# Kernel tuning notes

Hardware: AMD Instinct MI355X
Metric: run time of the kernel (lower is better)

## Reference

```python
import jax, jax.numpy as jnp
import numpy as np

N = 50000
E = 800000
H = 96
NUM_IN = 11
PE_DIM = 24
NUM_OUT = 1
NUM_LAYERS = 4
NUM_GRAPHS = 256


def _linear_params(key, d_in, d_out):
    k1, k2 = jax.random.split(key)
    bound = 1.0 / np.sqrt(d_in)
    w = jax.random.uniform(k1, (d_in, d_out), jnp.float32, -bound, bound)
    b = jax.random.uniform(k2, (d_out,), jnp.float32, -bound, bound)
    return w, b


def setup_inputs() -> dict:
    key = jax.random.key(0)
    ks = jax.random.split(key, 32)
    x = jax.random.normal(ks[0], (N, NUM_IN), jnp.float32)
    pos = jax.random.normal(ks[1], (N, 3), jnp.float32)
    pe = jax.random.normal(ks[2], (N, PE_DIM), jnp.float32)
    edge_index = jax.random.randint(ks[3], (2, E), 0, N, jnp.int64)
    batch = jnp.sort(jax.random.randint(ks[4], (N,), 0, NUM_GRAPHS, jnp.int64))
    embed_w1, embed_b1 = _linear_params(ks[5], NUM_IN + PE_DIM, H)
    embed_w2, embed_b2 = _linear_params(ks[6], H, H)
    # per-layer stacked params
    msg_w1 = []; msg_b1 = []; msg_w2 = []; msg_b2 = []
    upd_w1 = []; upd_b1 = []; upd_w2 = []; upd_b2 = []
    for l in range(NUM_LAYERS):
        w, b = _linear_params(ks[7 + l], 2 * H + 1, H); msg_w1.append(w); msg_b1.append(b)
        w, b = _linear_params(ks[11 + l], H, H); msg_w2.append(w); msg_b2.append(b)
        w, b = _linear_params(ks[15 + l], 2 * H, H); upd_w1.append(w); upd_b1.append(b)
        w, b = _linear_params(ks[19 + l], H, H); upd_w2.append(w); upd_b2.append(b)
    pre_w1, pre_b1 = _linear_params(ks[23], H, H)
    pre_w2, pre_b2 = _linear_params(ks[24], H, H)
    ro_w1, ro_b1 = _linear_params(ks[25], H, H)
    ro_w2, ro_b2 = _linear_params(ks[26], H, NUM_OUT)
    return {
        'x': x, 'pos': pos, 'pe': pe, 'edge_index': edge_index, 'batch': batch,
        'embed_w1': embed_w1, 'embed_b1': embed_b1, 'embed_w2': embed_w2, 'embed_b2': embed_b2,
        'msg_w1': jnp.stack(msg_w1), 'msg_b1': jnp.stack(msg_b1),
        'msg_w2': jnp.stack(msg_w2), 'msg_b2': jnp.stack(msg_b2),
        'upd_w1': jnp.stack(upd_w1), 'upd_b1': jnp.stack(upd_b1),
        'upd_w2': jnp.stack(upd_w2), 'upd_b2': jnp.stack(upd_b2),
        'pre_w1': pre_w1, 'pre_b1': pre_b1, 'pre_w2': pre_w2, 'pre_b2': pre_b2,
        'ro_w1': ro_w1, 'ro_b1': ro_b1, 'ro_w2': ro_w2, 'ro_b2': ro_b2,
    }


def _egnn_forward(x, pos, pe, edge_index, batch,
                  embed_w1, embed_b1, embed_w2, embed_b2,
                  msg_w1, msg_b1, msg_w2, msg_b2,
                  upd_w1, upd_b1, upd_w2, upd_b2,
                  pre_w1, pre_b1, pre_w2, pre_b2,
                  ro_w1, ro_b1, ro_w2, ro_b2):
    silu = jax.nn.silu
    send, rec = edge_index[0], edge_index[1]
    h = jnp.concatenate([x, pe], axis=-1)
    h = silu(h @ embed_w1 + embed_b1) @ embed_w2 + embed_b2  # [N,H]
    dist = jnp.linalg.norm(pos[send] - pos[rec], axis=1)[:, None]  # [E,1]
    for l in range(NUM_LAYERS):
        state = jnp.concatenate([h[send], h[rec], dist], axis=1)  # [E,2H+1]
        msg = silu(silu(state @ msg_w1[l] + msg_b1[l]) @ msg_w2[l] + msg_b2[l])  # [E,H]
        aggr = jax.ops.segment_sum(msg, rec, num_segments=h.shape[0])  # [N,H]
        upd_in = jnp.concatenate([h, aggr], axis=1)
        update = silu(upd_in @ upd_w1[l] + upd_b1[l]) @ upd_w2[l] + upd_b2[l]
        h = h + update
    h = silu(h @ pre_w1 + pre_b1) @ pre_w2 + pre_b2
    pooled = jax.ops.segment_sum(h, batch, num_segments=NUM_GRAPHS)  # [G,H]
    out = silu(pooled @ ro_w1 + ro_b1) @ ro_w2 + ro_b2  # [G,1]
    return jnp.squeeze(out)


def reference(x, pos, pe, edge_index, batch,
              embed_w1, embed_b1, embed_w2, embed_b2,
              msg_w1, msg_b1, msg_w2, msg_b2,
              upd_w1, upd_b1, upd_w2, upd_b2,
              pre_w1, pre_b1, pre_w2, pre_b2,
              ro_w1, ro_b1, ro_w2, ro_b2):
    return _egnn_forward(x, pos, pe, edge_index, batch,
                         embed_w1, embed_b1, embed_w2, embed_b2,
                         msg_w1, msg_b1, msg_w2, msg_b2,
                         upd_w1, upd_b1, upd_w2, upd_b2,
                         pre_w1, pre_b1, pre_w2, pre_b2,
                         ro_w1, ro_b1, ro_w2, ro_b2)
```

## Files before the change

kernel.cpp:

```cpp
#include <hip/hip_runtime.h>
#include <hip/hip_bf16.h>

#define HDIM 96
#define TILE 128
#define NTILE 64

typedef __attribute__((ext_vector_type(8))) short  short8;
typedef __attribute__((ext_vector_type(4))) short  short4v;
typedef __attribute__((ext_vector_type(4))) float  float4v;
typedef __attribute__((ext_vector_type(4))) unsigned int uint4v;

static __device__ __forceinline__ short f2bf(float f){
    unsigned u = __float_as_uint(f);
    return (short)((u + 0x8000u) >> 16);
}
static __device__ __forceinline__ float bf2f(short s){
    unsigned u = ((unsigned)(unsigned short)s) << 16;
    return __uint_as_float(u);
}
static __device__ __forceinline__ float silu_f(float v){
    return v * __builtin_amdgcn_rcpf(1.0f + __expf(-v));
}

struct SwJob { const float* src; int ck; int ks; int ksrc; };
struct SwTable { SwJob j[22]; };

__global__ __launch_bounds__(256) void swizzle_kernel(SwTable T, short* __restrict__ dst, int total){
    int gid = blockIdx.x*256 + threadIdx.x;
    if (gid >= total) return;
    int ksg = gid / 3072;
    int e   = gid % 3072;
    const float* src = T.j[0].src; int k0 = 0, ksrc = 0;
    #pragma unroll
    for (int jj = 0; jj < 22; ++jj){
        int s = T.j[jj].ck;
        if (ksg >= s && ksg < s + T.j[jj].ks){ src = T.j[jj].src; k0 = (ksg - s)*32; ksrc = T.j[jj].ksrc; }
    }
    int nt   = e >> 9;
    int rem  = e & 511;
    int lane = rem >> 3;
    int jx   = rem & 7;
    int k = k0 + ((lane >> 4) << 3) + jx;
    int f = nt*16 + (lane & 15);
    float v = (k < ksrc) ? src[(size_t)k*HDIM + f] : 0.0f;
    dst[gid] = f2bf(v);
}

__global__ __launch_bounds__(256) void swizzle2_kernel(const float* __restrict__ msg_w1,
                                                       short* __restrict__ dst, int total){
    int gid = blockIdx.x*256 + threadIdx.x;
    if (gid >= total) return;
    int layer = gid / 18432;
    int e     = gid % 18432;
    int ksg = e / 6144;
    int rem = e % 6144;
    int nt   = rem >> 9;
    int r2   = rem & 511;
    int lane = r2 >> 3;
    int jx   = r2 & 7;
    int k = ksg*32 + ((lane >> 4) << 3) + jx;
    int f = nt*16 + (lane & 15);
    int row = (f < 96) ? k : (96 + k);
    int col = (f < 96) ? f : (f - 96);
    dst[gid] = f2bf(msg_w1[(size_t)layer*193*96 + (size_t)row*96 + col]);
}

__global__ __launch_bounds__(256) void hist_kernel(const int* __restrict__ rec, int* __restrict__ deg, int E){
    int e = blockIdx.x*256 + threadIdx.x;
    if (e < E) atomicAdd(&deg[rec[e]], 1);
}

__global__ __launch_bounds__(256) void scan_part(const int* __restrict__ deg, int* __restrict__ part, int N){
    __shared__ int red[256];
    const int t = threadIdx.x;
    int base = blockIdx.x*1024;
    int s = 0;
    #pragma unroll
    for (int j=0;j<4;j++){ int i = base + j*256 + t; s += (i<N)?deg[i]:0; }
    red[t]=s; __syncthreads();
    #pragma unroll
    for (int off=128; off>0; off>>=1){ if (t<off) red[t]+=red[t+off]; __syncthreads(); }
    if (t==0) part[blockIdx.x]=red[0];
}
__global__ __launch_bounds__(256) void scan_top(int* __restrict__ part, int nb){
    __shared__ int buf[256];
    const int t = threadIdx.x;
    int v = (t < nb) ? part[t] : 0;
    buf[t] = v;
    __syncthreads();
    #pragma unroll
    for (int off=1; off<256; off<<=1){
        int u = (t>=off)?buf[t-off]:0;
        __syncthreads();
        buf[t] += u;
        __syncthreads();
    }
    if (t < nb) part[t] = buf[t] - v;
}
__global__ __launch_bounds__(256) void scan_final(const int* __restrict__ deg, const int* __restrict__ part,
                                                  int* __restrict__ cur, int N){
    __shared__ int tsum[256];
    const int t = threadIdx.x;
    int i0 = blockIdx.x*1024 + t*4;
    int a0 = (i0+0<N)?deg[i0+0]:0;
    int a1 = (i0+1<N)?deg[i0+1]:0;
    int a2 = (i0+2<N)?deg[i0+2]:0;
    int a3 = (i0+3<N)?deg[i0+3]:0;
    int s = a0+a1+a2+a3;
    tsum[t]=s; __syncthreads();
    #pragma unroll
    for (int off=1; off<256; off<<=1){
        int u = (t>=off)?tsum[t-off]:0;
        __syncthreads();
        tsum[t]+=u;
        __syncthreads();
    }
    int excl = tsum[t]-s + part[blockIdx.x];
    if (i0+0<N) cur[i0+0]=excl;
    if (i0+1<N) cur[i0+1]=excl+a0;
    if (i0+2<N) cur[i0+2]=excl+a0+a1;
    if (i0+3<N) cur[i0+3]=excl+a0+a1+a2;
}

__global__ __launch_bounds__(256) void scatter_kernel(
    const int* __restrict__ send, const int* __restrict__ rec, const float* __restrict__ pos,
    int* __restrict__ cur, int2* __restrict__ sd_s, int* __restrict__ rec_s, int E)
{
    int e = blockIdx.x*256 + threadIdx.x;
    if (e >= E) return;
    int s = send[e], r = rec[e];
    int p = atomicAdd(&cur[r], 1);
    float dx = pos[3*s]   - pos[3*r];
    float dy = pos[3*s+1] - pos[3*r+1];
    float dz = pos[3*s+2] - pos[3*r+2];
    float d = sqrtf(dx*dx + dy*dy + dz*dz);
    sd_s[p] = make_int2(s, __float_as_int(d));
    rec_s[p] = r;
}

__global__ __launch_bounds__(256,5) void edge_kernel(
    const short* __restrict__ SR,
    const int2* __restrict__ sd_s, const int* __restrict__ rec_s,
    const float* __restrict__ w1r192,
    const short* __restrict__ w2sw, const float* __restrict__ b2,
    float* __restrict__ aggr, int E)
{
    __shared__ short msgS[TILE*104];
    __shared__ int   recS[TILE];
    __shared__ int   startIdxS[TILE+1];
    __shared__ int   wcntS[2];
    const int t  = threadIdx.x;
    const int e0 = blockIdx.x * TILE;

    if (t < TILE) {
        int e = e0 + t; if (e >= E) e = E - 1;
        recS[t] = rec_s[e];
    }
    __syncthreads();

    bool flag = false;
    if (t < TILE) flag = (t == 0) || (recS[t] != recS[t-1]);
    unsigned long long bmask = __ballot(flag ? 1 : 0);
    int pre = __popcll(bmask & ((1ull << (t & 63)) - 1ull));
    if (t < TILE && (t & 63) == 0) wcntS[t >> 6] = __popcll(bmask);
    __syncthreads();
    const int nseg = wcntS[0] + wcntS[1];
    if (flag) startIdxS[pre + ((t >> 6) ? wcntS[0] : 0)] = t;
    if (t == 0) startIdxS[nseg] = TILE;

    const bool firstB = (e0 > 0) && (rec_s[e0-1] == recS[0]);
    const bool lastB  = (e0 + TILE < E) && (rec_s[e0 + TILE] == recS[TILE-1]);

    const int lane = t & 63;
    const int wv   = t >> 6;
    const int e_lo = wv * 32;
    const int col  = lane & 15;
    const int quad = lane >> 4;
    const int frow = quad * 4;
    const float4v fzero = {0.f,0.f,0.f,0.f};

    short8 frag[2][3];
    #pragma unroll
    for (int et=0; et<2; ++et){
        int ei = e_lo + et*16 + col;
        int ec = e0 + ei; if (ec >= E) ec = E - 1;
        int2 sd = sd_s[ec];
        int se = sd.x;
        float d = __int_as_float(sd.y);
        int re = recS[ei];
        #pragma unroll
        for (int ks=0; ks<3; ++ks){
            int f0 = ks*32 + quad*8;
            short8 S8 = *(const short8*)(SR + (size_t)se*192 + f0);
            short8 R8 = *(const short8*)(SR + (size_t)re*192 + 96 + f0);
            float4v wa = *(const float4v*)(w1r192 + f0);
            float4v wb = *(const float4v*)(w1r192 + f0 + 4);
            short8 fr;
            #pragma unroll
            for (int j=0;j<8;j++){
                float w = (j<4) ? wa[j] : wb[j-4];
                float v = bf2f(S8[j]) + bf2f(R8[j]) + d*w;
                fr[j] = f2bf(silu_f(v));
            }
            frag[et][ks] = fr;
        }
    }

    float4v acc2[2][6];
    #pragma unroll
    for (int i=0;i<2;i++)
      #pragma unroll
      for (int n=0;n<6;n++) acc2[i][n] = fzero;

    const short8* w2f = (const short8*)w2sw;
    #pragma unroll
    for (int ks = 0; ks < 3; ++ks) {
        #pragma unroll
        for (int mt = 0; mt < 6; ++mt) {
            short8 a = w2f[(ks*6+mt)*64 + lane];
            acc2[0][mt] = __builtin_amdgcn_mfma_f32_16x16x32_bf16(a, frag[0][ks], acc2[0][mt], 0, 0, 0);
            acc2[1][mt] = __builtin_amdgcn_mfma_f32_16x16x32_bf16(a, frag[1][ks], acc2[1][mt], 0, 0, 0);
        }
    }
    float4v b2v[6];
    #pragma unroll
    for (int mt=0; mt<6; ++mt) b2v[mt] = *(const float4v*)(b2 + mt*16 + frow);

    #pragma unroll
    for (int et=0; et<2; ++et){
        int e = e_lo + et*16 + col;
        bool valid = (e0 + e) < E;
        #pragma unroll
        for (int mt=0; mt<6; ++mt){
            short4v sv;
            #pragma unroll
            for (int r=0;r<4;r++){
                float u = silu_f(acc2[et][mt][r] + b2v[mt][r]);
                sv[r] = f2bf(valid ? u : 0.0f);
            }
            *(short4v*)(msgS + e*104 + mt*16 + frow) = sv;
        }
    }
    __syncthreads();

    const int items = nseg * 12;
    for (int item = t; item < items; item += 256){
        int s  = item / 12;
        int fg = item - s*12;
        int r0 = startIdxS[s], r1 = startIdxS[s+1];
        float sum[8] = {0.f,0.f,0.f,0.f,0.f,0.f,0.f,0.f};
        for (int r = r0; r < r1; ++r){
            short8 v8 = *(const short8*)(msgS + r*104 + fg*8);
            #pragma unroll
            for (int j=0;j<8;j++) sum[j] += bf2f(v8[j]);
        }
        float* dstp = aggr + (size_t)recS[r0]*HDIM + fg*8;
        bool bnd = (s == 0 && firstB) || (s == nseg-1 && lastB);
        if (bnd) {
            #pragma unroll
            for (int j=0;j<8;j++) atomicAdd(dstp+j, sum[j]);
        } else {
            float4v lo = {sum[0], sum[1], sum[2], sum[3]};
            float4v hi = {sum[4], sum[5], sum[6], sum[7]};
            *(float4v*)(dstp)     = lo;
            *(float4v*)(dstp + 4) = hi;
        }
    }
}

__global__ __launch_bounds__(128,3) void update_kernel(
    float* __restrict__ h, short* __restrict__ hbf, float* __restrict__ aggr,
    const short* __restrict__ w1sw, const float* __restrict__ b1,
    const short* __restrict__ w2sw, const float* __restrict__ b2,
    const short* __restrict__ w1sr_next, const float* __restrict__ msgb1_next,
    short* __restrict__ SR, int N)
{
    __shared__ short stateS[NTILE*200];
    const int t  = threadIdx.x;
    const int n0 = blockIdx.x * NTILE;

    #pragma unroll
    for (int it = 0; it < 12; ++it) {
        int q = it*128 + t;
        int c = q % 24;
        int i = q / 24;
        int node = n0 + i;
        if (c < 12) {
            uint4v v = {0u,0u,0u,0u};
            if (node < N) v = *(const uint4v*)(hbf + (size_t)node*HDIM + c*8);
            *(uint4v*)(stateS + i*200 + c*8) = v;
        } else {
            int cc = c - 12;
            short8 s8 = {0,0,0,0,0,0,0,0};
            if (node < N) {
                float4v a0 = *(const float4v*)(aggr + (size_t)node*HDIM + cc*8);
                float4v a1 = *(const float4v*)(aggr + (size_t)node*HDIM + cc*8 + 4);
                s8[0]=f2bf(a0[0]); s8[1]=f2bf(a0[1]); s8[2]=f2bf(a0[2]); s8[3]=f2bf(a0[3]);
                s8[4]=f2bf(a1[0]); s8[5]=f2bf(a1[1]); s8[6]=f2bf(a1[2]); s8[7]=f2bf(a1[3]);
            }
            *(short8*)(stateS + i*200 + HDIM + cc*8) = s8;
        }
    }
    __syncthreads();

    const int lane = t & 63;
    const int wv   = t >> 6;
    const int e_lo = wv * 32;
    const int col  = lane & 15;
    const int quad = lane >> 4;
    const int koff = quad * 8;
    const int frow = quad * 4;
    const float4v fzero = {0.f,0.f,0.f,0.f};

    float4v acc[2][6];
    #pragma unroll
    for (int i=0;i<2;i++)
      #pragma unroll
      for (int n=0;n<6;n++) acc[i][n] = fzero;

    const short8* w1f = (const short8*)w1sw;
    #pragma unroll
    for (int ks = 0; ks < 6; ++ks) {
        short8 bb0 = *(const short8*)(stateS + (e_lo+col)*200    + ks*32 + koff);
        short8 bb1 = *(const short8*)(stateS + (e_lo+16+col)*200 + ks*32 + koff);
        #pragma unroll
        for (int mt = 0; mt < 6; ++mt) {
            short8 a = w1f[(ks*6+mt)*64 + lane];
            acc[0][mt] = __builtin_amdgcn_mfma_f32_16x16x32_bf16(a, bb0, acc[0][mt], 0, 0, 0);
            acc[1][mt] = __builtin_amdgcn_mfma_f32_16x16x32_bf16(a, bb1, acc[1][mt], 0, 0, 0);
        }
    }
    float4v b1v[6];
    #pragma unroll
    for (int mt=0; mt<6; ++mt) b1v[mt] = *(const float4v*)(b1 + mt*16 + frow);
    __syncthreads();

    short* t1S = stateS;
    #pragma unroll
    for (int et=0; et<2; ++et){
        int e = e_lo + et*16 + col;
        #pragma unroll
        for (int mt=0; mt<6; ++mt){
            short4v sv;
            #pragma unroll
            for (int r=0;r<4;r++) sv[r] = f2bf(silu_f(acc[et][mt][r] + b1v[mt][r]));
            *(short4v*)(t1S + e*104 + mt*16 + frow) = sv;
        }
    }
    __syncthreads();

    float4v acc2[2][6];
    #pragma unroll
    for (int i=0;i<2;i++)
      #pragma unroll
      for (int n=0;n<6;n++) acc2[i][n] = fzero;

    const short8* w2f = (const short8*)w2sw;
    #pragma unroll
    for (int ks = 0; ks < 3; ++ks) {
        short8 bb0 = *(const short8*)(t1S + (e_lo+col)*104    + ks*32 + koff);
        short8 bb1 = *(const short8*)(t1S + (e_lo+16+col)*104 + ks*32 + koff);
        #pragma unroll
        for (int mt = 0; mt < 6; ++mt) {
            short8 a = w2f[(ks*6+mt)*64 + lane];
            acc2[0][mt] = __builtin_amdgcn_mfma_f32_16x16x32_bf16(a, bb0, acc2[0][mt], 0, 0, 0);
            acc2[1][mt] = __builtin_amdgcn_mfma_f32_16x16x32_bf16(a, bb1, acc2[1][mt], 0, 0, 0);
        }
    }
    float4v b2v[6];
    #pragma unroll
    for (int mt=0; mt<6; ++mt) b2v[mt] = *(const float4v*)(b2 + mt*16 + frow);
    __syncthreads();

    #pragma unroll
    for (int et=0; et<2; ++et){
        int erow = e_lo + et*16 + col;
        int node = n0 + erow;
        bool valid = node < N;
        size_t base = (size_t)node*HDIM;
        #pragma unroll
        for (int mt=0; mt<6; ++mt){
            int f0 = mt*16 + frow;
            float4v old = valid ? *(const float4v*)(h + base + f0) : fzero;
            float4v o;
            #pragma unroll
            for (int r=0;r<4;r++) o[r] = old[r] + acc2[et][mt][r] + b2v[mt][r];
            short4v sv = {f2bf(o[0]), f2bf(o[1]), f2bf(o[2]), f2bf(o[3])};
            if (valid) {
                *(float4v*)(h + base + f0) = o;
                *(short4v*)(hbf + base + f0) = sv;
                *(float4v*)(aggr + base + f0) = fzero;
            }
            *(short4v*)(stateS + erow*104 + f0) = sv;
        }
    }

    if (w1sr_next) {
        __syncthreads();
        float4v accS[2][12];
        #pragma unroll
        for (int i=0;i<2;i++)
          #pragma unroll
          for (int n=0;n<12;n++) accS[i][n] = fzero;

        const short8* wsf = (const short8*)w1sr_next;
        #pragma unroll
        for (int ks = 0; ks < 3; ++ks) {
            short8 bb0 = *(const short8*)(stateS + (e_lo+col)*104    + ks*32 + koff);
            short8 bb1 = *(const short8*)(stateS + (e_lo+16+col)*104 + ks*32 + koff);
            #pragma unroll
            for (int mt = 0; mt < 12; ++mt) {
                short8 a = wsf[(ks*12+mt)*64 + lane];
                accS[0][mt] = __builtin_amdgcn_mfma_f32_16x16x32_bf16(a, bb0, accS[0][mt], 0, 0, 0);
                accS[1][mt] = __builtin_amdgcn_mfma_f32_16x16x32_bf16(a, bb1, accS[1][mt], 0, 0, 0);
            }
        }
        float4v bnv[6];
        #pragma unroll
        for (int mt=0; mt<6; ++mt) bnv[mt] = *(const float4v*)(msgb1_next + mt*16 + frow);

        #pragma unroll
        for (int et=0; et<2; ++et){
            int node = n0 + e_lo + et*16 + col;
            if (node < N) {
                size_t sbase = (size_t)node*192;
                #pragma unroll
                for (int mt=0; mt<12; ++mt){
                    float4v o = accS[et][mt];
                    if (mt < 6) { o[0]+=bnv[mt][0]; o[1]+=bnv[mt][1]; o[2]+=bnv[mt][2]; o[3]+=bnv[mt][3]; }
                    short4v sv = {f2bf(o[0]), f2bf(o[1]), f2bf(o[2]), f2bf(o[3])};
                    *(short4v*)(SR + sbase + mt*16 + frow) = sv;
                }
            }
        }
    }
}

__global__ __launch_bounds__(128,3) void embed_kernel(
    const float* __restrict__ x, const float* __restrict__ pe,
    const short* __restrict__ w1sw, const float* __restrict__ b1,
    const short* __restrict__ w2sw, const float* __restrict__ b2,
    float* __restrict__ h, short* __restrict__ hbf,
    const short* __restrict__ w1sr0, const float* __restrict__ msgb1_0,
    short* __restrict__ SR, int N)
{
    __shared__ short stateS[NTILE*72];
    __shared__ short t1S[NTILE*104];
    const int t  = threadIdx.x;
    const int n0 = blockIdx.x * NTILE;

    if (t < NTILE) {
        int node = n0 + t;
        short* row = stateS + t*72;
        if (node < N) {
            #pragma unroll
            for (int j=0;j<11;j++) row[j]    = f2bf(x[(size_t)node*11 + j]);
            #pragma unroll
            for (int j=0;j<24;j++) row[11+j] = f2bf(pe[(size_t)node*24 + j]);
            #pragma unroll
            for (int j=35;j<64;j++) row[j] = 0;
        } else {
            #pragma unroll
            for (int j=0;j<64;j++) row[j] = 0;
        }
    }
    __syncthreads();

    const int lane = t & 63;
    const int wv   = t >> 6;
    const int e_lo = wv * 32;
    const int col  = lane & 15;
    const int quad = lane >> 4;
    const int koff = quad * 8;
    const int frow = quad * 4;
    const float4v fzero = {0.f,0.f,0.f,0.f};

    float4v acc[2][6];
    #pragma unroll
    for (int i=0;i<2;i++)
      #pragma unroll
      for (int n=0;n<6;n++) acc[i][n] = fzero;

    const short8* w1f = (const short8*)w1sw;
    #pragma unroll
    for (int ks = 0; ks < 2; ++ks) {
        short8 bb0 = *(const short8*)(stateS + (e_lo+col)*72    + ks*32 + koff);
        short8 bb1 = *(const short8*)(stateS + (e_lo+16+col)*72 + ks*32 + koff);
        #pragma unroll
        for (int mt = 0; mt < 6; ++mt) {
            short8 a = w1f[(ks*6+mt)*64 + lane];
            acc[0][mt] = __builtin_amdgcn_mfma_f32_16x16x32_bf16(a, bb0, acc[0][mt], 0, 0, 0);
            acc[1][mt] = __builtin_amdgcn_mfma_f32_16x16x32_bf16(a, bb1, acc[1][mt], 0, 0, 0);
        }
    }
    float4v b1v[6];
    #pragma unroll
    for (int mt=0; mt<6; ++mt) b1v[mt] = *(const float4v*)(b1 + mt*16 + frow);

    #pragma unroll
    for (int et=0; et<2; ++et){
        int e = e_lo + et*16 + col;
        #pragma unroll
        for (int mt=0; mt<6; ++mt){
            short4v sv;
            #pragma unroll
            for (int r=0;r<4;r++) sv[r] = f2bf(silu_f(acc[et][mt][r] + b1v[mt][r]));
            *(short4v*)(t1S + e*104 + mt*16 + frow) = sv;
        }
    }
    __syncthreads();

    float4v acc2[2][6];
    #pragma unroll
    for (int i=0;i<2;i++)
      #pragma unroll
      for (int n=0;n<6;n++) acc2[i][n] = fzero;

    const short8* w2f = (const short8*)w2sw;
    #pragma unroll
    for (int ks = 0; ks < 3; ++ks) {
        short8 bb0 = *(const short8*)(t1S + (e_lo+col)*104    + ks*32 + koff);
        short8 bb1 = *(const short8*)(t1S + (e_lo+16+col)*104 + ks*32 + koff);
        #pragma unroll
        for (int mt = 0; mt < 6; ++mt) {
            short8 a = w2f[(ks*6+mt)*64 + lane];
            acc2[0][mt] = __builtin_amdgcn_mfma_f32_16x16x32_bf16(a, bb0, acc2[0][mt], 0, 0, 0);
            acc2[1][mt] = __builtin_amdgcn_mfma_f32_16x16x32_bf16(a, bb1, acc2[1][mt], 0, 0, 0);
        }
    }
    float4v b2v[6];
    #pragma unroll
    for (int mt=0; mt<6; ++mt) b2v[mt] = *(const float4v*)(b2 + mt*16 + frow);
    __syncthreads();

    #pragma unroll
    for (int et=0; et<2; ++et){
        int erow = e_lo + et*16 + col;
        int node = n0 + erow;
        bool valid = node < N;
        size_t base = (size_t)node*HDIM;
        #pragma unroll
        for (int mt=0; mt<6; ++mt){
            int f0 = mt*16 + frow;
            float4v o;
            #pragma unroll
            for (int r=0;r<4;r++) o[r] = acc2[et][mt][r] + b2v[mt][r];
            short4v sv = {f2bf(o[0]), f2bf(o[1]), f2bf(o[2]), f2bf(o[3])};
            if (valid) {
                *(float4v*)(h + base + f0) = o;
                *(short4v*)(hbf + base + f0) = sv;
            }
            *(short4v*)(t1S + erow*104 + f0) = sv;
        }
    }
    __syncthreads();

    float4v accS[2][12];
    #pragma unroll
    for (int i=0;i<2;i++)
      #pragma unroll
      for (int n=0;n<12;n++) accS[i][n] = fzero;

    const short8* wsf = (const short8*)w1sr0;
    #pragma unroll
    for (int ks = 0; ks < 3; ++ks) {
        short8 bb0 = *(const short8*)(t1S + (e_lo+col)*104    + ks*32 + koff);
        short8 bb1 = *(const short8*)(t1S + (e_lo+16+col)*104 + ks*32 + koff);
        #pragma unroll
        for (int mt = 0; mt < 12; ++mt) {
            short8 a = wsf[(ks*12+mt)*64 + lane];
            accS[0][mt] = __builtin_amdgcn_mfma_f32_16x16x32_bf16(a, bb0, accS[0][mt], 0, 0, 0);
            accS[1][mt] = __builtin_amdgcn_mfma_f32_16x16x32_bf16(a, bb1, accS[1][mt], 0, 0, 0);
        }
    }
    float4v bnv[6];
    #pragma unroll
    for (int mt=0; mt<6; ++mt) bnv[mt] = *(const float4v*)(msgb1_0 + mt*16 + frow);

    #pragma unroll
    for (int et=0; et<2; ++et){
        int node = n0 + e_lo + et*16 + col;
        if (node < N) {
            size_t sbase = (size_t)node*192;
            #pragma unroll
            for (int mt=0; mt<12; ++mt){
                float4v o = accS[et][mt];
                if (mt < 6) { o[0]+=bnv[mt][0]; o[1]+=bnv[mt][1]; o[2]+=bnv[mt][2]; o[3]+=bnv[mt][3]; }
                short4v sv = {f2bf(o[0]), f2bf(o[1]), f2bf(o[2]), f2bf(o[3])};
                *(short4v*)(SR + sbase + mt*16 + frow) = sv;
            }
        }
    }
}

__global__ __launch_bounds__(128,3) void prepool_kernel(
    const short* __restrict__ hbf,
    const short* __restrict__ w1sw, const float* __restrict__ b1,
    const short* __restrict__ w2sw, const float* __restrict__ b2,
    const int* __restrict__ batch, float* __restrict__ pooled, int N)
{
    __shared__ short bufS[NTILE*104*2];
    __shared__ int   batchS[NTILE];
    __shared__ int   startIdxS[NTILE+1];
    __shared__ int   nsegS;
    short* stateS = bufS;
    short* t1S    = bufS + NTILE*104;
    float* msgS   = (float*)bufS;
    const int t  = threadIdx.x;
    const int n0 = blockIdx.x * NTILE;

    #pragma unroll
    for (int it = 0; it < 6; ++it) {
        int q = it*128 + t;
        int c = q % 12;
        int i = q / 12;
        int node = n0 + i;
        uint4v v = {0u,0u,0u,0u};
        if (node < N) v = *(const uint4v*)(hbf + (size_t)node*HDIM + c*8);
        *(uint4v*)(stateS + i*104 + c*8) = v;
    }
    if (t < NTILE) {
        int node = n0 + t;
        batchS[t] = batch[node < N ? node : N-1];
    }
    __syncthreads();

    bool flag = false;
    if (t < NTILE) flag = (t == 0) || (batchS[t] != batchS[t-1]);
    unsigned long long bmask = __ballot(flag ? 1 : 0);
    if (t < NTILE) {
        int pre = __popcll(bmask & ((1ull << t) - 1ull));
        if (flag) startIdxS[pre] = t;
        if (t == 0) nsegS = __popcll(bmask);
    }

    const int lane = t & 63;
    const int wv   = t >> 6;
    const int e_lo = wv * 32;
    const int col  = lane & 15;
    const int quad = lane >> 4;
    const int koff = quad * 8;
    const int frow = quad * 4;
    const float4v fzero = {0.f,0.f,0.f,0.f};

    float4v acc[2][6];
    #pragma unroll
    for (int i=0;i<2;i++)
      #pragma unroll
      for (int n=0;n<6;n++) acc[i][n] = fzero;

    const short8* w1f = (const short8*)w1sw;
    #pragma unroll
    for (int ks = 0; ks < 3; ++ks) {
        short8 bb0 = *(const short8*)(stateS + (e_lo+col)*104    + ks*32 + koff);
        short8 bb1 = *(const short8*)(stateS + (e_lo+16+col)*104 + ks*32 + koff);
        #pragma unroll
        for (int mt = 0; mt < 6; ++mt) {
            short8 a = w1f[(ks*6+mt)*64 + lane];
            acc[0][mt] = __builtin_amdgcn_mfma_f32_16x16x32_bf16(a, bb0, acc[0][mt], 0, 0, 0);
            acc[1][mt] = __builtin_amdgcn_mfma_f32_16x16x32_bf16(a, bb1, acc[1][mt], 0, 0, 0);
        }
    }
    float4v b1v[6];
    #pragma unroll
    for (int mt=0; mt<6; ++mt) b1v[mt] = *(const float4v*)(b1 + mt*16 + frow);

    #pragma unroll
    for (int et=0; et<2; ++et){
        int e = e_lo + et*16 + col;
        #pragma unroll
        for (int mt=0; mt<6; ++mt){
            short4v sv;
            #pragma unroll
            for (int r=0;r<4;r++) sv[r] = f2bf(silu_f(acc[et][mt][r] + b1v[mt][r]));
            *(short4v*)(t1S + e*104 + mt*16 + frow) = sv;
        }
    }
    __syncthreads();
    const int nseg = nsegS;
    if (t == 0) startIdxS[nseg] = NTILE;

    float4v acc2[2][6];
    #pragma unroll
    for (int i=0;i<2;i++)
      #pragma unroll
      for (int n=0;n<6;n++) acc2[i][n] = fzero;

    const short8* w2f = (const short8*)w2sw;
    #pragma unroll
    for (int ks = 0; ks < 3; ++ks) {
        short8 bb0 = *(const short8*)(t1S + (e_lo+col)*104    + ks*32 + koff);
        short8 bb1 = *(const short8*)(t1S + (e_lo+16+col)*104 + ks*32 + koff);
        #pragma unroll
        for (int mt = 0; mt < 6; ++mt) {
            short8 a = w2f[(ks*6+mt)*64 + lane];
            acc2[0][mt] = __builtin_amdgcn_mfma_f32_16x16x32_bf16(a, bb0, acc2[0][mt], 0, 0, 0);
            acc2[1][mt] = __builtin_amdgcn_mfma_f32_16x16x32_bf16(a, bb1, acc2[1][mt], 0, 0, 0);
        }
    }
    float4v b2v[6];
    #pragma unroll
    for (int mt=0; mt<6; ++mt) b2v[mt] = *(const float4v*)(b2 + mt*16 + frow);
    __syncthreads();

    #pragma unroll
    for (int et=0; et<2; ++et){
        int e = e_lo + et*16 + col;
        bool valid = (n0 + e) < N;
        #pragma unroll
        for (int mt=0; mt<6; ++mt){
            float4v v;
            #pragma unroll
            for (int r=0;r<4;r++){
                float u = acc2[et][mt][r] + b2v[mt][r];
                v[r] = valid ? u : 0.0f;
            }
            *(float4v*)(msgS + e*100 + mt*16 + frow) = v;
        }
    }
    __syncthreads();

    const int items = nseg * 24;
    for (int item = t; item < items; item += 128){
        int s  = item / 24;
        int fg = item - s*24;
        int r0 = startIdxS[s], r1 = startIdxS[s+1];
        float4v sum = fzero;
        for (int r = r0; r < r1; ++r) sum += *(const float4v*)(msgS + r*100 + fg*4);
        float* dstp = pooled + (size_t)batchS[r0]*HDIM + fg*4;
        atomicAdd(dstp+0, sum[0]);
        atomicAdd(dstp+1, sum[1]);
        atomicAdd(dstp+2, sum[2]);
        atomicAdd(dstp+3, sum[3]);
    }
}

__global__ __launch_bounds__(128) void readout_kernel(
    const float* __restrict__ pooled,
    const float* __restrict__ w1, const float* __restrict__ b1,
    const float* __restrict__ w2, const float* __restrict__ b2,
    float* __restrict__ out)
{
    __shared__ float red[128];
    const int g = blockIdx.x;
    const int t = threadIdx.x;
    float p = 0.0f;
    if (t < HDIM) {
        float acc = b1[t];
        for (int k = 0; k < HDIM; ++k)
            acc += pooled[(size_t)g*HDIM + k] * w1[(size_t)k*HDIM + t];
        acc = silu_f(acc);
        p = acc * w2[t];
    }
    red[t] = p;
    __syncthreads();
    for (int s = 64; s > 0; s >>= 1) {
        if (t < s) red[t] += red[t + s];
        __syncthreads();
    }
    if (t == 0) out[g] = red[0] + b2[0];
}

extern "C" void kernel_launch(void* const* d_in, const int* in_sizes, int n_in,
                              void* d_out, int out_size, void* d_ws, size_t ws_size,
                              hipStream_t stream)
{
    const float* x        = (const float*)d_in[0];
    const float* pos      = (const float*)d_in[1];
    const float* pe       = (const float*)d_in[2];
    const int*   ei       = (const int*)d_in[3];
    const int*   batch    = (const int*)d_in[4];
    const float* embed_w1 = (const float*)d_in[5];
    const float* embed_b1 = (const float*)d_in[6];
    const float* embed_w2 = (const float*)d_in[7];
    const float* embed_b2 = (const float*)d_in[8];
    const float* msg_w1   = (const float*)d_in[9];
    const float* msg_b1   = (const float*)d_in[10];
    const float* msg_w2   = (const float*)d_in[11];
    const float* msg_b2   = (const float*)d_in[12];
    const float* upd_w1   = (const float*)d_in[13];
    const float* upd_b1   = (const float*)d_in[14];
    const float* upd_w2   = (const float*)d_in[15];
    const float* upd_b2   = (const float*)d_in[16];
    const float* pre_w1   = (const float*)d_in[17];
    const float* pre_b1   = (const float*)d_in[18];
    const float* pre_w2   = (const float*)d_in[19];
    const float* pre_b2   = (const float*)d_in[20];
    const float* ro_w1    = (const float*)d_in[21];
    const float* ro_b1    = (const float*)d_in[22];
    const float* ro_w2    = (const float*)d_in[23];
    const float* ro_b2    = (const float*)d_in[24];

    const int E = in_sizes[3] / 2;
    const int N = in_sizes[4];
    const int G = out_size;

    char* ws = (char*)d_ws;
    size_t off = 0;
    auto alloc = [&](size_t bytes){ void* p = ws + off; off += (bytes + 255) & ~(size_t)255; return p; };
    float* h      = (float*)alloc((size_t)N*HDIM*4);
    short* hbf    = (short*)alloc((size_t)N*HDIM*2);
    float* aggr   = (float*)alloc((size_t)N*HDIM*4);
    float* pooled = (float*)alloc((size_t)G*HDIM*4);
    short* wsw    = (short*)alloc((size_t)59*3072*2);
    short* w1sr   = (short*)alloc((size_t)4*18432*2);
    short* SR     = (short*)alloc((size_t)N*192*2);
    int*   deg    = (int*)alloc((size_t)N*4);
    int*   cur    = (int*)alloc((size_t)N*4);
    int*   part   = (int*)alloc((size_t)256*4);
    int2*  sd_s   = (int2*)alloc((size_t)E*8);
    int*   rec_s  = (int*)alloc((size_t)E*4);

    hipMemsetAsync(aggr,   0, (size_t)N*HDIM*4, stream);
    hipMemsetAsync(pooled, 0, (size_t)G*HDIM*4, stream);
    hipMemsetAsync(deg,    0, (size_t)N*4, stream);

    SwTable T;
    for (int jj=0;jj<22;jj++){ T.j[jj].src = embed_w1; T.j[jj].ck = 1<<30; T.j[jj].ks = 0; T.j[jj].ksrc = 0; }
    int ck = 0, ji = 0;
    auto add = [&](const float* s, int ks, int ksrc){
        T.j[ji].src = s; T.j[ji].ck = ck; T.j[ji].ks = ks; T.j[ji].ksrc = ksrc;
        ji++; ck += ks;
    };
    add(embed_w1, 2, 35);
    add(embed_w2, 3, 96);
    add(pre_w1,   3, 96);
    add(pre_w2,   3, 96);
    for (int l=0;l<4;l++) add(msg_w2 + (size_t)l*96*96,  3, 96);
    for (int l=0;l<4;l++) add(upd_w1 + (size_t)l*192*96, 6, 192);
    for (int l=0;l<4;l++) add(upd_w2 + (size_t)l*96*96,  3, 96);
    const int total = 59*3072;
    swizzle_kernel<<<(total+255)/256, 256, 0, stream>>>(T, wsw, total);
    const int total2 = 4*18432;
    swizzle2_kernel<<<(total2+255)/256, 256, 0, stream>>>(msg_w1, w1sr, total2);

    const int nbE256 = (E + 255) / 256;
    const int nbScan = (N + 1023) / 1024;
    hist_kernel<<<nbE256, 256, 0, stream>>>(ei + E, deg, E);
    scan_part<<<nbScan, 256, 0, stream>>>(deg, part, N);
    scan_top<<<1, 256, 0, stream>>>(part, nbScan);
    scan_final<<<nbScan, 256, 0, stream>>>(deg, part, cur, N);
    scatter_kernel<<<nbE256, 256, 0, stream>>>(ei, ei + E, pos, cur, sd_s, rec_s, E);

    const int nbN = (N + NTILE - 1) / NTILE;
    embed_kernel<<<nbN, 128, 0, stream>>>(x, pe, wsw + 0, embed_b1, wsw + 2*3072, embed_b2,
                                          h, hbf, w1sr, msg_b1, SR, N);

    const int nbE = (E + TILE - 1) / TILE;
    for (int l = 0; l < 4; ++l) {
        edge_kernel<<<nbE, 256, 0, stream>>>(SR, sd_s, rec_s,
            msg_w1 + (size_t)l*193*96 + (size_t)192*96,
            wsw + (11 + 3*l)*3072, msg_b2 + l*96, aggr, E);
        const short* w1sr_next = (l < 3) ? (w1sr + (size_t)(l+1)*18432) : nullptr;
        const float* msgb1_next = (l < 3) ? (msg_b1 + (l+1)*96) : nullptr;
        update_kernel<<<nbN, 128, 0, stream>>>(h, hbf, aggr,
            wsw + (23 + 6*l)*3072, upd_b1 + l*96,
            wsw + (47 + 3*l)*3072, upd_b2 + l*96,
            w1sr_next, msgb1_next, SR, N);
    }

    prepool_kernel<<<nbN, 128, 0, stream>>>(hbf, wsw + 5*3072, pre_b1, wsw + 8*3072, pre_b2,
                                            batch, pooled, N);
    readout_kernel<<<G, 128, 0, stream>>>(pooled, ro_w1, ro_b1, ro_w2, ro_b2, (float*)d_out);
}
```

Measured before the change: 803.0 us.

## Fuse prepool into last update kernel, merge swizzles, prefetch edge gathers early

Folds the pre-pooling MLP and the graph segment-sum into the last layer's update kernel, so the final node state never goes back to memory and one launch is removed. The two weight-swizzle kernels are merged into a single launch. The edge kernel now issues its sender and receiver feature gathers before the segment-boundary setup and its barrier, so those loads can overlap with that work. In exchange the update kernel uses more shared memory and registers, which may lower its occupancy in every layer.

```diff
diff --git a/kernel.cpp b/kernel.cpp
--- a/kernel.cpp
+++ b/kernel.cpp
@@ -25,44 +25,43 @@
 struct SwJob { const float* src; int ck; int ks; int ksrc; };
 struct SwTable { SwJob j[22]; };
 
-__global__ __launch_bounds__(256) void swizzle_kernel(SwTable T, short* __restrict__ dst, int total){
+__global__ __launch_bounds__(256) void swizzle_all(SwTable T, const float* __restrict__ msg_w1,
+                                                   short* __restrict__ dst, short* __restrict__ dst2,
+                                                   int total1, int total2){
     int gid = blockIdx.x*256 + threadIdx.x;
-    if (gid >= total) return;
-    int ksg = gid / 3072;
-    int e   = gid % 3072;
-    const float* src = T.j[0].src; int k0 = 0, ksrc = 0;
-    #pragma unroll
-    for (int jj = 0; jj < 22; ++jj){
-        int s = T.j[jj].ck;
-        if (ksg >= s && ksg < s + T.j[jj].ks){ src = T.j[jj].src; k0 = (ksg - s)*32; ksrc = T.j[jj].ksrc; }
-    }
-    int nt   = e >> 9;
-    int rem  = e & 511;
-    int lane = rem >> 3;
-    int jx   = rem & 7;
-    int k = k0 + ((lane >> 4) << 3) + jx;
-    int f = nt*16 + (lane & 15);
-    float v = (k < ksrc) ? src[(size_t)k*HDIM + f] : 0.0f;
-    dst[gid] = f2bf(v);
-}
-
-__global__ __launch_bounds__(256) void swizzle2_kernel(const float* __restrict__ msg_w1,
-                                                       short* __restrict__ dst, int total){
-    int gid = blockIdx.x*256 + threadIdx.x;
-    if (gid >= total) return;
-    int layer = gid / 18432;
-    int e     = gid % 18432;
-    int ksg = e / 6144;
-    int rem = e % 6144;
-    int nt   = rem >> 9;
-    int r2   = rem & 511;
-    int lane = r2 >> 3;
-    int jx   = r2 & 7;
-    int k = ksg*32 + ((lane >> 4) << 3) + jx;
-    int f = nt*16 + (lane & 15);
-    int row = (f < 96) ? k : (96 + k);
-    int col = (f < 96) ? f : (f - 96);
-    dst[gid] = f2bf(msg_w1[(size_t)layer*193*96 + (size_t)row*96 + col]);
+    if (gid < total1) {
+        int ksg = gid / 3072;
+        int e   = gid % 3072;
+        const float* src = T.j[0].src; int k0 = 0, ksrc = 0;
+        #pragma unroll
+        for (int jj = 0; jj < 22; ++jj){
+            int s = T.j[jj].ck;
+            if (ksg >= s && ksg < s + T.j[jj].ks){ src = T.j[jj].src; k0 = (ksg - s)*32; ksrc = T.j[jj].ksrc; }
+        }
+        int nt   = e >> 9;
+        int rem  = e & 511;
+        int lane = rem >> 3;
+        int jx   = rem & 7;
+        int k = k0 + ((lane >> 4) << 3) + jx;
+        int f = nt*16 + (lane & 15);
+        float v = (k < ksrc) ? src[(size_t)k*HDIM + f] : 0.0f;
+        dst[gid] = f2bf(v);
+    } else if (gid < total1 + total2) {
+        int g2 = gid - total1;
+        int layer = g2 / 18432;
+        int e     = g2 % 18432;
+        int ksg = e / 6144;
+        int rem = e % 6144;
+        int nt   = rem >> 9;
+        int r2   = rem & 511;
+        int lane = r2 >> 3;
+        int jx   = r2 & 7;
+        int k = ksg*32 + ((lane >> 4) << 3) + jx;
+        int f = nt*16 + (lane & 15);
+        int row = (f < 96) ? k : (96 + k);
+        int col = (f < 96) ? f : (f - 96);
+        dst2[g2] = f2bf(msg_w1[(size_t)layer*193*96 + (size_t)row*96 + col]);
+    }
 }
 
 __global__ __launch_bounds__(256) void hist_kernel(const int* __restrict__ rec, int* __restrict__ deg, int E){
@@ -151,26 +150,6 @@
     __shared__ int   wcntS[2];
     const int t  = threadIdx.x;
     const int e0 = blockIdx.x * TILE;
-
-    if (t < TILE) {
-        int e = e0 + t; if (e >= E) e = E - 1;
-        recS[t] = rec_s[e];
-    }
-    __syncthreads();
-
-    bool flag = false;
-    if (t < TILE) flag = (t == 0) || (recS[t] != recS[t-1]);
-    unsigned long long bmask = __ballot(flag ? 1 : 0);
-    int pre = __popcll(bmask & ((1ull << (t & 63)) - 1ull));
-    if (t < TILE && (t & 63) == 0) wcntS[t >> 6] = __popcll(bmask);
-    __syncthreads();
-    const int nseg = wcntS[0] + wcntS[1];
-    if (flag) startIdxS[pre + ((t >> 6) ? wcntS[0] : 0)] = t;
-    if (t == 0) startIdxS[nseg] = TILE;
-
-    const bool firstB = (e0 > 0) && (rec_s[e0-1] == recS[0]);
-    const bool lastB  = (e0 + TILE < E) && (rec_s[e0 + TILE] == recS[TILE-1]);
-
     const int lane = t & 63;
     const int wv   = t >> 6;
     const int e_lo = wv * 32;
@@ -179,22 +158,55 @@
     const int frow = quad * 4;
     const float4v fzero = {0.f,0.f,0.f,0.f};
 
+    int se[2], re[2]; float dd[2];
+    #pragma unroll
+    for (int et=0; et<2; ++et){
+        int ec = e0 + e_lo + et*16 + col; if (ec >= E) ec = E - 1;
+        int2 sd = sd_s[ec];
+        se[et] = sd.x; dd[et] = __int_as_float(sd.y);
+        re[et] = rec_s[ec];
+    }
+    short8 Sv[2][3], Rv[2][3];
+    #pragma unroll
+    for (int et=0; et<2; ++et)
+      #pragma unroll
+      for (int ks=0; ks<3; ++ks){
+        int f0 = ks*32 + quad*8;
+        Sv[et][ks] = *(const short8*)(SR + (size_t)se[et]*192 + f0);
+        Rv[et][ks] = *(const short8*)(SR + (size_t)re[et]*192 + 96 + f0);
+      }
+
+    int myRec = 0;
+    bool flag = false;
+    if (t < TILE) {
+        int e = e0 + t; if (e >= E) e = E - 1;
+        myRec = rec_s[e];
+        recS[t] = myRec;
+        int ep = e0 + t - 1; if (ep >= E) ep = E - 1;
+        flag = (t == 0) || (myRec != rec_s[ep]);
+    }
+    unsigned long long bmask = __ballot(flag ? 1 : 0);
+    int pre = __popcll(bmask & ((1ull << (t & 63)) - 1ull));
+    if (t < TILE && (t & 63) == 0) wcntS[t >> 6] = __popcll(bmask);
+
+    const bool firstB = (e0 > 0) && (rec_s[e0-1] == rec_s[e0]);
+    const bool lastB  = (e0 + TILE < E) && (rec_s[e0 + TILE] == rec_s[(e0+TILE-1 < E)? e0+TILE-1 : E-1]);
+
+    __syncthreads();
+
+    if (flag) startIdxS[pre + ((t >> 6) ? wcntS[0] : 0)] = t;
+    if (t == 0) startIdxS[wcntS[0] + wcntS[1]] = TILE;
+
     short8 frag[2][3];
     #pragma unroll
     for (int et=0; et<2; ++et){
-        int ei = e_lo + et*16 + col;
-        int ec = e0 + ei; if (ec >= E) ec = E - 1;
-        int2 sd = sd_s[ec];
-        int se = sd.x;
-        float d = __int_as_float(sd.y);
-        int re = recS[ei];
+        float d = dd[et];
         #pragma unroll
         for (int ks=0; ks<3; ++ks){
             int f0 = ks*32 + quad*8;
-            short8 S8 = *(const short8*)(SR + (size_t)se*192 + f0);
-            short8 R8 = *(const short8*)(SR + (size_t)re*192 + 96 + f0);
             float4v wa = *(const float4v*)(w1r192 + f0);
             float4v wb = *(const float4v*)(w1r192 + f0 + 4);
+            short8 S8 = Sv[et][ks], R8 = Rv[et][ks];
             short8 fr;
             #pragma unroll
             for (int j=0;j<8;j++){
@@ -243,6 +255,7 @@
     }
     __syncthreads();
 
+    const int nseg = wcntS[0] + wcntS[1];
     const int items = nseg * 12;
     for (int item = t; item < items; item += 256){
         int s  = item / 12;
@@ -273,9 +286,15 @@
     const short* __restrict__ w1sw, const float* __restrict__ b1,
     const short* __restrict__ w2sw, const float* __restrict__ b2,
     const short* __restrict__ w1sr_next, const float* __restrict__ msgb1_next,
-    short* __restrict__ SR, int N)
+    short* __restrict__ SR,
+    const short* __restrict__ pw1, const float* __restrict__ pb1,
+    const short* __restrict__ pw2, const float* __restrict__ pb2,
+    const int* __restrict__ batch, float* __restrict__ pooled, int N)
 {
-    __shared__ short stateS[NTILE*200];
+    __shared__ short stateS[NTILE*208];
+    __shared__ int   batchS[NTILE];
+    __shared__ int   startIdxS[NTILE+1];
+    __shared__ int   nsegS;
     const int t  = threadIdx.x;
     const int n0 = blockIdx.x * NTILE;
 
@@ -433,6 +452,116 @@
                 }
             }
         }
+    } else if (pw1) {
+        if (t < NTILE) {
+            int node = n0 + t;
+            batchS[t] = batch[node < N ? node : N-1];
+        }
+        __syncthreads();
+
+        bool flag = false;
+        if (t < NTILE) flag = (t == 0) || (batchS[t] != batchS[t-1]);
+        unsigned long long bm = __ballot(flag ? 1 : 0);
+        if (t < NTILE) {
+            int pre = __popcll(bm & ((1ull << t) - 1ull));
+            if (flag) startIdxS[pre] = t;
+            if (t == 0) nsegS = __popcll(bm);
+        }
+
+        float4v accp[2][6];
+        #pragma unroll
+        for (int i=0;i<2;i++)
+          #pragma unroll
+          for (int n=0;n<6;n++) accp[i][n] = fzero;
+
+        const short8* pw1f = (const short8*)pw1;
+        #pragma unroll
+        for (int ks = 0; ks < 3; ++ks) {
+            short8 bb0 = *(const short8*)(stateS + (e_lo+col)*104    + ks*32 + koff);
+            short8 bb1 = *(const short8*)(stateS + (e_lo+16+col)*104 + ks*32 + koff);
+            #pragma unroll
+            for (int mt = 0; mt < 6; ++mt) {
+                short8 a = pw1f[(ks*6+mt)*64 + lane];
+                accp[0][mt] = __builtin_amdgcn_mfma_f32_16x16x32_bf16(a, bb0, accp[0][mt], 0, 0, 0);
+                accp[1][mt] = __builtin_amdgcn_mfma_f32_16x16x32_bf16(a, bb1, accp[1][mt], 0, 0, 0);
+            }
+        }
+        float4v pb1v[6];
+        #pragma unroll
+        for (int mt=0; mt<6; ++mt) pb1v[mt] = *(const float4v*)(pb1 + mt*16 + frow);
+
+        short* t1p = stateS + NTILE*104;
+        #pragma unroll
+        for (int et=0; et<2; ++et){
+            int e = e_lo + et*16 + col;
+            #pragma unroll
+            for (int mt=0; mt<6; ++mt){
+                short4v sv;
+                #pragma unroll
+                for (int r=0;r<4;r++) sv[r] = f2bf(silu_f(accp[et][mt][r] + pb1v[mt][r]));
+                *(short4v*)(t1p + e*104 + mt*16 + frow) = sv;
+            }
+        }
+        __syncthreads();
+
+        float4v accq[2][6];
+        #pragma unroll
+        for (int i=0;i<2;i++)
+          #pragma unroll
+          for (int n=0;n<6;n++) accq[i][n] = fzero;
+
+        const short8* pw2f = (const short8*)pw2;
+        #pragma unroll
+        for (int ks = 0; ks < 3; ++ks) {
+            short8 bb0 = *(const short8*)(t1p + (e_lo+col)*104    + ks*32 + koff);
+            short8 bb1 = *(const short8*)(t1p + (e_lo+16+col)*104 + ks*32 + koff);
+            #pragma unroll
+            for (int mt = 0; mt < 6; ++mt) {
+                short8 a = pw2f[(ks*6+mt)*64 + lane];
+                accq[0][mt] = __builtin_amdgcn_mfma_f32_16x16x32_bf16(a, bb0, accq[0][mt], 0, 0, 0);
+                accq[1][mt] = __builtin_amdgcn_mfma_f32_16x16x32_bf16(a, bb1, accq[1][mt], 0, 0, 0);
+            }
+        }
+        float4v pb2v[6];
+        #pragma unroll
+        for (int mt=0; mt<6; ++mt) pb2v[mt] = *(const float4v*)(pb2 + mt*16 + frow);
+        __syncthreads();
+
+        float* msgS = (float*)stateS;
+        #pragma unroll
+        for (int et=0; et<2; ++et){
+            int e = e_lo + et*16 + col;
+            bool valid = (n0 + e) < N;
+            #pragma unroll
+            for (int mt=0; mt<6; ++mt){
+                float4v v;
+                #pragma unroll
+                for (int r=0;r<4;r++){
+                    float u = accq[et][mt][r] + pb2v[mt][r];
+                    v[r] = valid ? u : 0.0f;
+                }
+                *(float4v*)(msgS + e*100 + mt*16 + frow) = v;
+            }
+        }
+        __syncthreads();
+
+        const int nseg = nsegS;
+        if (t == 0) startIdxS[nseg] = NTILE;
+        __syncthreads();
+
+        const int items = nseg * 24;
+        for (int item = t; item < items; item += 128){
+            int s  = item / 24;
+            int fg = item - s*24;
+            int r0 = startIdxS[s], r1 = startIdxS[s+1];
+            float4v sum = fzero;
+            for (int r = r0; r < r1; ++r) sum += *(const float4v*)(msgS + r*100 + fg*4);
+            float* dstp = pooled + (size_t)batchS[r0]*HDIM + fg*4;
+            atomicAdd(dstp+0, sum[0]);
+            atomicAdd(dstp+1, sum[1]);
+            atomicAdd(dstp+2, sum[2]);
+            atomicAdd(dstp+3, sum[3]);
+        }
     }
 }
 
@@ -590,148 +719,6 @@
                 *(short4v*)(SR + sbase + mt*16 + frow) = sv;
             }
         }
-    }
-}
-
-__global__ __launch_bounds__(128,3) void prepool_kernel(
-    const short* __restrict__ hbf,
-    const short* __restrict__ w1sw, const float* __restrict__ b1,
-    const short* __restrict__ w2sw, const float* __restrict__ b2,
-    const int* __restrict__ batch, float* __restrict__ pooled, int N)
-{
-    __shared__ short bufS[NTILE*104*2];
-    __shared__ int   batchS[NTILE];
-    __shared__ int   startIdxS[NTILE+1];
-    __shared__ int   nsegS;
-    short* stateS = bufS;
-    short* t1S    = bufS + NTILE*104;
-    float* msgS   = (float*)bufS;
-    const int t  = threadIdx.x;
-    const int n0 = blockIdx.x * NTILE;
-
-    #pragma unroll
-    for (int it = 0; it < 6; ++it) {
-        int q = it*128 + t;
-        int c = q % 12;
-        int i = q / 12;
-        int node = n0 + i;
-        uint4v v = {0u,0u,0u,0u};
-        if (node < N) v = *(const uint4v*)(hbf + (size_t)node*HDIM + c*8);
-        *(uint4v*)(stateS + i*104 + c*8) = v;
-    }
-    if (t < NTILE) {
-        int node = n0 + t;
-        batchS[t] = batch[node < N ? node : N-1];
-    }
-    __syncthreads();
-
-    bool flag = false;
-    if (t < NTILE) flag = (t == 0) || (batchS[t] != batchS[t-1]);
-    unsigned long long bmask = __ballot(flag ? 1 : 0);
-    if (t < NTILE) {
-        int pre = __popcll(bmask & ((1ull << t) - 1ull));
-        if (flag) startIdxS[pre] = t;
-        if (t == 0) nsegS = __popcll(bmask);
-    }
-
-    const int lane = t & 63;
-    const int wv   = t >> 6;
-    const int e_lo = wv * 32;
-    const int col  = lane & 15;
-    const int quad = lane >> 4;
-    const int koff = quad * 8;
-    const int frow = quad * 4;
-    const float4v fzero = {0.f,0.f,0.f,0.f};
-
-    float4v acc[2][6];
-    #pragma unroll
-    for (int i=0;i<2;i++)
-      #pragma unroll
-      for (int n=0;n<6;n++) acc[i][n] = fzero;
-
-    const short8* w1f = (const short8*)w1sw;
-    #pragma unroll
-    for (int ks = 0; ks < 3; ++ks) {
-        short8 bb0 = *(const short8*)(stateS + (e_lo+col)*104    + ks*32 + koff);
-        short8 bb1 = *(const short8*)(stateS + (e_lo+16+col)*104 + ks*32 + koff);
-        #pragma unroll
-        for (int mt = 0; mt < 6; ++mt) {
-            short8 a = w1f[(ks*6+mt)*64 + lane];
-            acc[0][mt] = __builtin_amdgcn_mfma_f32_16x16x32_bf16(a, bb0, acc[0][mt], 0, 0, 0);
-            acc[1][mt] = __builtin_amdgcn_mfma_f32_16x16x32_bf16(a, bb1, acc[1][mt], 0, 0, 0);
-        }
-    }
-    float4v b1v[6];
-    #pragma unroll
-    for (int mt=0; mt<6; ++mt) b1v[mt] = *(const float4v*)(b1 + mt*16 + frow);
-
-    #pragma unroll
-    for (int et=0; et<2; ++et){
-        int e = e_lo + et*16 + col;
-        #pragma unroll
-        for (int mt=0; mt<6; ++mt){
-            short4v sv;
-            #pragma unroll
-            for (int r=0;r<4;r++) sv[r] = f2bf(silu_f(acc[et][mt][r] + b1v[mt][r]));
-            *(short4v*)(t1S + e*104 + mt*16 + frow) = sv;
-        }
-    }
-    __syncthreads();
-    const int nseg = nsegS;
-    if (t == 0) startIdxS[nseg] = NTILE;
-
-    float4v acc2[2][6];
-    #pragma unroll
-    for (int i=0;i<2;i++)
-      #pragma unroll
-      for (int n=0;n<6;n++) acc2[i][n] = fzero;
-
-    const short8* w2f = (const short8*)w2sw;
-    #pragma unroll
-    for (int ks = 0; ks < 3; ++ks) {
-        short8 bb0 = *(const short8*)(t1S + (e_lo+col)*104    + ks*32 + koff);
-        short8 bb1 = *(const short8*)(t1S + (e_lo+16+col)*104 + ks*32 + koff);
-        #pragma unroll
-        for (int mt = 0; mt < 6; ++mt) {
-            short8 a = w2f[(ks*6+mt)*64 + lane];
-            acc2[0][mt] = __builtin_amdgcn_mfma_f32_16x16x32_bf16(a, bb0, acc2[0][mt], 0, 0, 0);
-            acc2[1][mt] = __builtin_amdgcn_mfma_f32_16x16x32_bf16(a, bb1, acc2[1][mt], 0, 0, 0);
-        }
-    }
-    float4v b2v[6];
-    #pragma unroll
-    for (int mt=0; mt<6; ++mt) b2v[mt] = *(const float4v*)(b2 + mt*16 + frow);
-    __syncthreads();
-
-    #pragma unroll
-    for (int et=0; et<2; ++et){
-        int e = e_lo + et*16 + col;
-        bool valid = (n0 + e) < N;
-        #pragma unroll
-        for (int mt=0; mt<6; ++mt){
-            float4v v;
-            #pragma unroll
-            for (int r=0;r<4;r++){
-                float u = acc2[et][mt][r] + b2v[mt][r];
-                v[r] = valid ? u : 0.0f;
-            }
-            *(float4v*)(msgS + e*100 + mt*16 + frow) = v;
-        }
-    }
-    __syncthreads();
-
-    const int items = nseg * 24;
-    for (int item = t; item < items; item += 128){
-        int s  = item / 24;
-        int fg = item - s*24;
-        int r0 = startIdxS[s], r1 = startIdxS[s+1];
-        float4v sum = fzero;
-        for (int r = r0; r < r1; ++r) sum += *(const float4v*)(msgS + r*100 + fg*4);
-        float* dstp = pooled + (size_t)batchS[r0]*HDIM + fg*4;
-        atomicAdd(dstp+0, sum[0]);
-        atomicAdd(dstp+1, sum[1]);
-        atomicAdd(dstp+2, sum[2]);
-        atomicAdd(dstp+3, sum[3]);
     }
 }
 
@@ -829,10 +816,9 @@
     for (int l=0;l<4;l++) add(msg_w2 + (size_t)l*96*96,  3, 96);
     for (int l=0;l<4;l++) add(upd_w1 + (size_t)l*192*96, 6, 192);
     for (int l=0;l<4;l++) add(upd_w2 + (size_t)l*96*96,  3, 96);
-    const int total = 59*3072;
-    swizzle_kernel<<<(total+255)/256, 256, 0, stream>>>(T, wsw, total);
+    const int total1 = 59*3072;
     const int total2 = 4*18432;
-    swizzle2_kernel<<<(total2+255)/256, 256, 0, stream>>>(msg_w1, w1sr, total2);
+    swizzle_all<<<(total1+total2+255)/256, 256, 0, stream>>>(T, msg_w1, wsw, w1sr, total1, total2);
 
     const int nbE256 = (E + 255) / 256;
     const int nbScan = (N + 1023) / 1024;
@@ -851,15 +837,18 @@
         edge_kernel<<<nbE, 256, 0, stream>>>(SR, sd_s, rec_s,
             msg_w1 + (size_t)l*193*96 + (size_t)192*96,
             wsw + (11 + 3*l)*3072, msg_b2 + l*96, aggr, E);
-        const short* w1sr_next = (l < 3) ? (w1sr + (size_t)(l+1)*18432) : nullptr;
+        const short* w1sr_next  = (l < 3) ? (w1sr + (size_t)(l+1)*18432) : nullptr;
         const float* msgb1_next = (l < 3) ? (msg_b1 + (l+1)*96) : nullptr;
+        const short* pw1 = (l == 3) ? (wsw + 5*3072) : nullptr;
+        const float* pb1 = (l == 3) ? pre_b1 : nullptr;
+        const short* pw2 = (l == 3) ? (wsw + 8*3072) : nullptr;
+        const float* pb2 = (l == 3) ? pre_b2 : nullptr;
         update_kernel<<<nbN, 128, 0, stream>>>(h, hbf, aggr,
             wsw + (23 + 6*l)*3072, upd_b1 + l*96,
             wsw + (47 + 3*l)*3072, upd_b2 + l*96,
-            w1sr_next, msgb1_next, SR, N);
-    }
-
-    prepool_kernel<<<nbN, 128, 0, stream>>>(hbf, wsw + 5*3072, pre_b1, wsw + 8*3072, pre_b2,
-                                            batch, pooled, N);
+            w1sr_next, msgb1_next, SR,
+            pw1, pb1, pw2, pb2, batch, pooled, N);
+    }
+
     readout_kernel<<<G, 128, 0, stream>>>(pooled, ro_w1, ro_b1, ro_w2, ro_b2, (float*)d_out);
 }
```

After: 753.6 us. 1.07x faster.
